# Optimization experiments

Measured on AMD Instinct MI355X. Metric: run time of the kernel, lower is better.

Reference implementation:

```python
import jax, jax.numpy as jnp
import numpy as np

NUM_NODES = 32
GNN_OBS_DIM = 16   # obs_dim // num_nodes
ACT_DIM = 2        # gnn_action_dim = action_dim // num_nodes
LOG_STD_MIN, LOG_STD_MAX = -5.0, 2.0


def _build_edges(bs):
    # complete graph per sample (undirected -> both directions), offset by i*N per batch,
    # plus self-loops (GCNConv add_self_loops=True). Static, built with numpy.
    n = NUM_NODES
    ii, jj = np.meshgrid(np.arange(n), np.arange(n), indexing='ij')
    mask = ii != jj
    s0, d0 = ii[mask], jj[mask]                      # [n*(n-1)]
    off = (np.arange(bs) * n)[:, None]
    src = (s0[None, :] + off).reshape(-1)
    dst = (d0[None, :] + off).reshape(-1)
    loop = np.arange(bs * n)
    src = np.concatenate([src, loop])
    dst = np.concatenate([dst, loop])
    return jnp.asarray(src, jnp.int32), jnp.asarray(dst, jnp.int32)


def _gcn_layer(x, W, b, src, dst, norm, num_seg):
    # GCNConv: out_i = sum_j norm_ij * (x_j W) + b, symmetric normalization, self-loops included.
    h = x @ W                                   # small GEMM
    msg = h[src] * norm[:, None]                # edge gather (memory bound)
    out = jax.ops.segment_sum(msg, dst, num_segments=num_seg)
    return out + b


def reference(obs, W1, b1, W2, b2, Wm1, bm1, Wm2, bm2):
    bs = obs.shape[0]
    nn_total = bs * NUM_NODES
    x = obs.reshape(nn_total, GNN_OBS_DIM)
    # robot_loc = x[:, :ACT_DIM] is only used for edge weights, which the source
    # overwrites with ones (edge_weights = torch.ones_like(edge_weights)).
    feat = x[:, ACT_DIM:]                        # [bs*N, 14]

    src, dst = _build_edges(bs)
    ew = jnp.ones(src.shape[0], dtype=obs.dtype)
    deg = jax.ops.segment_sum(ew, dst, num_segments=nn_total)
    dinv = jax.lax.rsqrt(deg)
    norm = dinv[src] * dinv[dst]                 # symmetric GCN normalization

    h = jax.nn.relu(_gcn_layer(feat, W1, b1, src, dst, norm, nn_total))
    h = jax.nn.relu(_gcn_layer(h, W2, b2, src, dst, norm, nn_total))

    # output MLP head
    m = jax.nn.relu(h @ Wm1 + bm1)
    out = m @ Wm2 + bm2                          # [bs*N, 2*ACT_DIM]

    mu, log_std = out[:, :ACT_DIM], out[:, ACT_DIM:]
    mu = mu.reshape(bs, -1)
    log_std = jnp.tanh(log_std.reshape(bs, -1))
    log_std = LOG_STD_MIN + 0.5 * (LOG_STD_MAX - LOG_STD_MIN) * (log_std + 1.0)
    std = jnp.exp(log_std)
    # SquashedNormal(mu, std) params; return them stacked: [2, bs, action_dim]
    return jnp.stack([mu, std])


def setup_inputs() -> dict:
    key = jax.random.key(0)
    ks = jax.random.split(key, 6)
    sc = 0.1
    return {
        'obs': jax.random.normal(ks[0], (1024, 512), jnp.float32),
        'W1': jax.random.normal(ks[1], (14, 128), jnp.float32) * sc,
        'b1': jnp.zeros((128,), jnp.float32),
        'W2': jax.random.normal(ks[2], (128, 128), jnp.float32) * sc,
        'b2': jnp.zeros((128,), jnp.float32),
        'Wm1': jax.random.normal(ks[3], (128, 128), jnp.float32) * sc,
        'bm1': jnp.zeros((128,), jnp.float32),
        'Wm2': jax.random.normal(ks[4], (128, 4), jnp.float32) * sc,
        'bm2': jnp.zeros((4,), jnp.float32),
    }
```

## Files before the change

### kernel.cpp

```cpp
#include <hip/hip_runtime.h>
#include <math.h>


constexpr int NODES = 32;
constexpr int OBSD  = 16;
constexpr int FEAT  = 14;
constexpr int H     = 128;
constexpr int SPB   = 4;
constexpr int TPB   = 128;

__global__ __launch_bounds__(TPB) void gcn_actor(
    const float* __restrict__ obs,
    const float* __restrict__ W1,  const float* __restrict__ b1,
    const float* __restrict__ W2,  const float* __restrict__ b2,
    const float* __restrict__ Wm1, const float* __restrict__ bm1,
    const float* __restrict__ Wm2, const float* __restrict__ bm2,
    float* __restrict__ out, int bs)
{
    const int tid = threadIdx.x;
    const int s0  = blockIdx.x * SPB;

    __shared__ float s_obs[SPB * NODES * OBSD];
    __shared__ float s_mean[SPB][FEAT];
    __shared__ float s_ga[SPB][H];
    __shared__ float s_gb[SPB][H];
    __shared__ float s_o[SPB][4];

    {
        const float4* gsrc = reinterpret_cast<const float4*>(obs + (size_t)s0 * NODES * OBSD);
        float4* ldst = reinterpret_cast<float4*>(s_obs);
        #pragma unroll
        for (int i = 0; i < (SPB * NODES * OBSD / 4) / TPB; ++i)
            ldst[tid + i * TPB] = gsrc[tid + i * TPB];
    }
    __syncthreads();

    if (tid < SPB * FEAT) {
        const int s = tid / FEAT, c = tid % FEAT;
        float acc = 0.f;
        const float* p = s_obs + s * NODES * OBSD + 2 + c;
        #pragma unroll
        for (int n = 0; n < NODES; ++n) acc += p[n * OBSD];
        s_mean[s][c] = acc * (1.0f / NODES);
    }
    __syncthreads();

    {
        float acc[SPB];
        const float bb = b1[tid];
        #pragma unroll
        for (int s = 0; s < SPB; ++s) acc[s] = bb;
        #pragma unroll
        for (int k = 0; k < FEAT; ++k) {
            const float w = W1[k * H + tid];
            #pragma unroll
            for (int s = 0; s < SPB; ++s) acc[s] = fmaf(w, s_mean[s][k], acc[s]);
        }
        #pragma unroll
        for (int s = 0; s < SPB; ++s) s_ga[s][tid] = fmaxf(acc[s], 0.f);
    }
    __syncthreads();

    {
        float acc[SPB];
        const float bb = b2[tid];
        #pragma unroll
        for (int s = 0; s < SPB; ++s) acc[s] = bb;
        #pragma unroll 8
        for (int k = 0; k < H; ++k) {
            const float w = W2[k * H + tid];
            #pragma unroll
            for (int s = 0; s < SPB; ++s) acc[s] = fmaf(w, s_ga[s][k], acc[s]);
        }
        #pragma unroll
        for (int s = 0; s < SPB; ++s) s_gb[s][tid] = fmaxf(acc[s], 0.f);
    }
    __syncthreads();

    {
        float acc[SPB];
        const float bb = bm1[tid];
        #pragma unroll
        for (int s = 0; s < SPB; ++s) acc[s] = bb;
        #pragma unroll 8
        for (int k = 0; k < H; ++k) {
            const float w = Wm1[k * H + tid];
            #pragma unroll
            for (int s = 0; s < SPB; ++s) acc[s] = fmaf(w, s_gb[s][k], acc[s]);
        }
        #pragma unroll
        for (int s = 0; s < SPB; ++s) s_ga[s][tid] = fmaxf(acc[s], 0.f);
    }
    __syncthreads();

    if (tid < SPB * 4) {
        const int s = tid / 4, c = tid % 4;
        float acc = bm2[c];
        #pragma unroll 8
        for (int k = 0; k < H; ++k) acc = fmaf(s_ga[s][k], Wm2[k * 4 + c], acc);
        if (c >= 2) {
            const float t  = tanhf(acc);
            const float ls = -5.0f + 3.5f * (t + 1.0f);
            acc = expf(ls);
        }
        s_o[s][c] = acc;
    }
    __syncthreads();

    {
        const int half = tid >> 6;
        const int t    = tid & 63;
        const int s    = t >> 4;
        const float v0 = s_o[s][half * 2 + 0];
        const float v1 = s_o[s][half * 2 + 1];
        float4* dst = reinterpret_cast<float4*>(out + (size_t)half * bs * 64 + (size_t)s0 * 64);
        dst[t] = make_float4(v0, v1, v0, v1);
    }
}

extern "C" void kernel_launch(void* const* d_in, const int* in_sizes, int n_in,
                              void* d_out, int out_size, void* d_ws, size_t ws_size,
                              hipStream_t stream) {
    const float* obs = (const float*)d_in[0];
    const float* W1  = (const float*)d_in[1];
    const float* b1  = (const float*)d_in[2];
    const float* W2  = (const float*)d_in[3];
    const float* b2  = (const float*)d_in[4];
    const float* Wm1 = (const float*)d_in[5];
    const float* bm1 = (const float*)d_in[6];
    const float* Wm2 = (const float*)d_in[7];
    const float* bm2 = (const float*)d_in[8];
    float* out = (float*)d_out;

    const int bs   = in_sizes[0] / (NODES * OBSD);
    const int grid = bs / SPB;

    gcn_actor<<<grid, TPB, 0, stream>>>(obs, W1, b1, W2, b2, Wm1, bm1, Wm2, bm2, out, bs);
}
```

Before: 84.49 us.

## Split K dimension across 512 threads with shared-memory partial-sum reductions

Raises the block size from 128 to 512 threads and splits each dense layer's K loop into four quarters, one per thread group, with partial sums reduced through shared memory. The node-mean and the final 128x4 head are also parallelized: the head uses a warp-shuffle reduction instead of 16 serial threads. The intent is to shorten the per-block serial latency chain. The cost is extra barriers, extra shared-memory traffic and larger blocks that may limit occupancy.

```diff
diff --git a/kernel.cpp b/kernel.cpp
--- a/kernel.cpp
+++ b/kernel.cpp
@@ -7,7 +7,7 @@
 constexpr int FEAT  = 14;
 constexpr int H     = 128;
 constexpr int SPB   = 4;
-constexpr int TPB   = 128;
+constexpr int TPB   = 512;
 
 __global__ __launch_bounds__(TPB) void gcn_actor(
     const float* __restrict__ obs,
@@ -19,95 +19,146 @@
 {
     const int tid = threadIdx.x;
     const int s0  = blockIdx.x * SPB;
+    const int n   = tid & (H - 1);
+    const int q   = tid >> 7;
 
     __shared__ float s_obs[SPB * NODES * OBSD];
     __shared__ float s_mean[SPB][FEAT];
-    __shared__ float s_ga[SPB][H];
-    __shared__ float s_gb[SPB][H];
+    __shared__ float s_part[4][SPB][H];
+    __shared__ float s_x[SPB][H];
+    __shared__ float s_y[SPB][H];
     __shared__ float s_o[SPB][4];
 
     {
-        const float4* gsrc = reinterpret_cast<const float4*>(obs + (size_t)s0 * NODES * OBSD);
-        float4* ldst = reinterpret_cast<float4*>(s_obs);
-        #pragma unroll
-        for (int i = 0; i < (SPB * NODES * OBSD / 4) / TPB; ++i)
-            ldst[tid + i * TPB] = gsrc[tid + i * TPB];
+        const float4* g = reinterpret_cast<const float4*>(obs + (size_t)s0 * NODES * OBSD);
+        reinterpret_cast<float4*>(s_obs)[tid] = g[tid];
     }
     __syncthreads();
 
+    if (tid < SPB * FEAT * 4) {
+        const int p = tid & 3, cs = tid >> 2;
+        const int s = cs / FEAT, c = cs - s * FEAT;
+        const float* base = s_obs + s * NODES * OBSD + 2 + c;
+        float a = 0.f;
+        #pragma unroll
+        for (int j = 0; j < 8; ++j) a += base[(p * 8 + j) * OBSD];
+        reinterpret_cast<float*>(s_part)[tid] = a;
+    }
+    __syncthreads();
     if (tid < SPB * FEAT) {
-        const int s = tid / FEAT, c = tid % FEAT;
-        float acc = 0.f;
-        const float* p = s_obs + s * NODES * OBSD + 2 + c;
+        float a = 0.f;
         #pragma unroll
-        for (int n = 0; n < NODES; ++n) acc += p[n * OBSD];
-        s_mean[s][c] = acc * (1.0f / NODES);
+        for (int p = 0; p < 4; ++p) a += reinterpret_cast<float*>(s_part)[tid * 4 + p];
+        const int s = tid / FEAT, c = tid - s * FEAT;
+        s_mean[s][c] = a * (1.0f / NODES);
     }
     __syncthreads();
 
     {
-        float acc[SPB];
-        const float bb = b1[tid];
-        #pragma unroll
-        for (int s = 0; s < SPB; ++s) acc[s] = bb;
-        #pragma unroll
-        for (int k = 0; k < FEAT; ++k) {
-            const float w = W1[k * H + tid];
+        float acc[SPB] = {0.f, 0.f, 0.f, 0.f};
+        const int k0 = q * 4;
+        const int kc = (FEAT - k0 < 4) ? (FEAT - k0) : 4;
+        for (int i = 0; i < kc; ++i) {
+            const int k = k0 + i;
+            const float w = W1[k * H + n];
             #pragma unroll
             for (int s = 0; s < SPB; ++s) acc[s] = fmaf(w, s_mean[s][k], acc[s]);
         }
         #pragma unroll
-        for (int s = 0; s < SPB; ++s) s_ga[s][tid] = fmaxf(acc[s], 0.f);
+        for (int s = 0; s < SPB; ++s) s_part[q][s][n] = acc[s];
+    }
+    __syncthreads();
+    {
+        const int s2 = tid >> 7, n2 = tid & (H - 1);
+        float v = b1[n2];
+        #pragma unroll
+        for (int qq = 0; qq < 4; ++qq) v += s_part[qq][s2][n2];
+        s_x[s2][n2] = fmaxf(v, 0.f);
     }
     __syncthreads();
 
     {
-        float acc[SPB];
-        const float bb = b2[tid];
+        float acc[SPB] = {0.f, 0.f, 0.f, 0.f};
+        const int kbase = q * 32;
         #pragma unroll
-        for (int s = 0; s < SPB; ++s) acc[s] = bb;
-        #pragma unroll 8
-        for (int k = 0; k < H; ++k) {
-            const float w = W2[k * H + tid];
+        for (int i = 0; i < 8; ++i) {
+            const int k = kbase + i * 4;
+            const float w0 = W2[(k + 0) * H + n];
+            const float w1 = W2[(k + 1) * H + n];
+            const float w2 = W2[(k + 2) * H + n];
+            const float w3 = W2[(k + 3) * H + n];
             #pragma unroll
-            for (int s = 0; s < SPB; ++s) acc[s] = fmaf(w, s_ga[s][k], acc[s]);
+            for (int s = 0; s < SPB; ++s) {
+                const float4 xv = *reinterpret_cast<const float4*>(&s_x[s][k]);
+                acc[s] = fmaf(w3, xv.w, fmaf(w2, xv.z, fmaf(w1, xv.y, fmaf(w0, xv.x, acc[s]))));
+            }
         }
         #pragma unroll
-        for (int s = 0; s < SPB; ++s) s_gb[s][tid] = fmaxf(acc[s], 0.f);
+        for (int s = 0; s < SPB; ++s) s_part[q][s][n] = acc[s];
+    }
+    __syncthreads();
+    {
+        const int s2 = tid >> 7, n2 = tid & (H - 1);
+        float v = b2[n2];
+        #pragma unroll
+        for (int qq = 0; qq < 4; ++qq) v += s_part[qq][s2][n2];
+        s_y[s2][n2] = fmaxf(v, 0.f);
     }
     __syncthreads();
 
     {
-        float acc[SPB];
-        const float bb = bm1[tid];
+        float acc[SPB] = {0.f, 0.f, 0.f, 0.f};
+        const int kbase = q * 32;
         #pragma unroll
-        for (int s = 0; s < SPB; ++s) acc[s] = bb;
-        #pragma unroll 8
-        for (int k = 0; k < H; ++k) {
-            const float w = Wm1[k * H + tid];
+        for (int i = 0; i < 8; ++i) {
+            const int k = kbase + i * 4;
+            const float w0 = Wm1[(k + 0) * H + n];
+            const float w1 = Wm1[(k + 1) * H + n];
+            const float w2 = Wm1[(k + 2) * H + n];
+            const float w3 = Wm1[(k + 3) * H + n];
             #pragma unroll
-            for (int s = 0; s < SPB; ++s) acc[s] = fmaf(w, s_gb[s][k], acc[s]);
+            for (int s = 0; s < SPB; ++s) {
+                const float4 xv = *reinterpret_cast<const float4*>(&s_y[s][k]);
+                acc[s] = fmaf(w3, xv.w, fmaf(w2, xv.z, fmaf(w1, xv.y, fmaf(w0, xv.x, acc[s]))));
+            }
         }
         #pragma unroll
-        for (int s = 0; s < SPB; ++s) s_ga[s][tid] = fmaxf(acc[s], 0.f);
+        for (int s = 0; s < SPB; ++s) s_part[q][s][n] = acc[s];
     }
     __syncthreads();
-
-    if (tid < SPB * 4) {
-        const int s = tid / 4, c = tid % 4;
-        float acc = bm2[c];
-        #pragma unroll 8
-        for (int k = 0; k < H; ++k) acc = fmaf(s_ga[s][k], Wm2[k * 4 + c], acc);
-        if (c >= 2) {
-            const float t  = tanhf(acc);
-            const float ls = -5.0f + 3.5f * (t + 1.0f);
-            acc = expf(ls);
-        }
-        s_o[s][c] = acc;
+    {
+        const int s2 = tid >> 7, n2 = tid & (H - 1);
+        float v = bm1[n2];
+        #pragma unroll
+        for (int qq = 0; qq < 4; ++qq) v += s_part[qq][s2][n2];
+        s_x[s2][n2] = fmaxf(v, 0.f);
     }
     __syncthreads();
 
     {
+        const int p5 = tid & 31;
+        const int c5 = (tid >> 5) & 3;
+        const int s5 = tid >> 7;
+        const float4 mv = reinterpret_cast<const float4*>(s_x[s5])[p5];
+        const int k = p5 * 4;
+        float acc = mv.x * Wm2[(k + 0) * 4 + c5];
+        acc = fmaf(mv.y, Wm2[(k + 1) * 4 + c5], acc);
+        acc = fmaf(mv.z, Wm2[(k + 2) * 4 + c5], acc);
+        acc = fmaf(mv.w, Wm2[(k + 3) * 4 + c5], acc);
+        #pragma unroll
+        for (int m = 16; m; m >>= 1) acc += __shfl_xor(acc, m, 64);
+        if (p5 == 0) {
+            float v = acc + bm2[c5];
+            if (c5 >= 2) {
+                const float t = tanhf(v);
+                v = expf(-5.0f + 3.5f * (t + 1.0f));
+            }
+            s_o[s5][c5] = v;
+        }
+    }
+    __syncthreads();
+
+    if (tid < 128) {
         const int half = tid >> 6;
         const int t    = tid & 63;
         const int s    = t >> 4;
```

Result: faster. 74.46 us (-11.9%).
